# Optimization experiments

Hardware: AMD Instinct MI355X
Metric: run time of the kernel (lower is better)

The kernel has to match this reference:

```python
import jax, jax.numpy as jnp
import numpy as np

N = 100000      # nodes
E = 400000      # edges
G = 4096        # graphs in batch
ATOM_DIM = 101
BOND_DIM = 11
D = 128         # latent_dim
L = 3           # num_atom_layers
BN_EPS = 1e-5


def setup_inputs() -> dict:
    key = jax.random.key(0)
    ks = jax.random.split(key, 16)
    x = jax.random.normal(ks[0], (N, ATOM_DIM), dtype=jnp.float32)
    edge_index = jax.random.randint(ks[1], (2, E), 0, N, dtype=jnp.int64)
    batch = jnp.sort(jax.random.randint(ks[2], (N,), 0, G, dtype=jnp.int64))
    edge_attr = jax.random.normal(ks[3], (E, BOND_DIM), dtype=jnp.float32)
    s = 0.05
    embW = jax.random.normal(ks[4], (ATOM_DIM, D), dtype=jnp.float32) * s
    embB = jnp.zeros((D,), dtype=jnp.float32)
    bondW = jax.random.normal(ks[5], (L, BOND_DIM, D), dtype=jnp.float32) * s
    bondB = jnp.zeros((L, D), dtype=jnp.float32)
    W1 = jax.random.normal(ks[6], (L, D, 2 * D), dtype=jnp.float32) * s
    b1 = jnp.zeros((L, 2 * D), dtype=jnp.float32)
    g1 = jnp.ones((L, 2 * D), dtype=jnp.float32)
    be1 = jnp.zeros((L, 2 * D), dtype=jnp.float32)
    W2 = jax.random.normal(ks[7], (L, 2 * D, D), dtype=jnp.float32) * s
    b2 = jnp.zeros((L, D), dtype=jnp.float32)
    gout = jnp.ones((L, D), dtype=jnp.float32)
    bout = jnp.zeros((L, D), dtype=jnp.float32)
    return dict(x=x, edge_attr=edge_attr, embW=embW, embB=embB,
                bondW=bondW, bondB=bondB, W1=W1, b1=b1, g1=g1, be1=be1,
                W2=W2, b2=b2, gout=gout, bout=bout,
                edge_index=edge_index, batch=batch)


def _bn(h, gamma, beta):
    # BatchNorm1d in training mode: batch stats over node axis, biased variance
    m = h.mean(axis=0)
    v = h.var(axis=0)
    return (h - m) * jax.lax.rsqrt(v + BN_EPS) * gamma + beta


def reference(x, edge_attr, embW, embB, bondW, bondB, W1, b1, g1, be1,
              W2, b2, gout, bout, edge_index, batch):
    src, dst = edge_index[0], edge_index[1]
    h = x @ embW + embB                              # [N, D]
    for i in range(L):
        e = edge_attr @ bondW[i] + bondB[i]          # [E, D] bond embedding
        msg = jax.nn.relu(h[src] + e)                # gather + add + relu
        agg = jax.ops.segment_sum(msg, dst, num_segments=N)  # scatter-add
        z = h + agg                                  # (1 + eps) * x + agg, eps = 0
        z = jax.nn.relu(_bn(z @ W1[i] + b1[i], g1[i], be1[i]))  # [N, 2D]
        h = z @ W2[i] + b2[i]                        # [N, D]
        h = _bn(h, gout[i], bout[i])
        if i != L - 1:
            h = jax.nn.relu(h)
    # global mean pool per graph
    sums = jax.ops.segment_sum(h, batch, num_segments=G)            # [G, D]
    cnts = jax.ops.segment_sum(jnp.ones((h.shape[0],), h.dtype), batch,
                               num_segments=G)
    return sums / jnp.maximum(cnts, 1.0)[:, None]
```

## Files before the change

kernel.cpp:

```cpp
#include <hip/hip_runtime.h>
#include <hip/hip_bf16.h>

#define NN 100000
#define EE 400000
#define GG 4096
#define DD 128
#define ATOM_DIM 101
#define BOND_DIM 11
#define EAP 12
#define GEMM_GRID 512

typedef __attribute__((ext_vector_type(8))) short bf16x8;
typedef __attribute__((ext_vector_type(4))) float f32x4;
typedef __attribute__((ext_vector_type(2))) float f32x2;

__device__ __forceinline__ float b2f(short s) {
    unsigned u = ((unsigned)(unsigned short)s) << 16;
    float f; __builtin_memcpy(&f, &u, 4); return f;
}
__device__ __forceinline__ unsigned short f2b(float f) {
    unsigned u; __builtin_memcpy(&u, &f, 4);
    u += 0x7FFFu + ((u >> 16) & 1u);
    return (unsigned short)(u >> 16);
}

__global__ void detect64_kernel(const void* ei, int npairs, int* flag) {
    const int* p = (const int*)ei;
    int any = 0;
    for (int i = 1; i < 2 * npairs; i += 2) any |= p[i];
    *flag = (any == 0) ? 1 : 0;
}
__device__ __forceinline__ int getIdx(const void* p, long i, int is64) {
    if (is64) return (int)(((const long long*)p)[i]);
    return ((const int*)p)[i];
}

__global__ __launch_bounds__(256) void hist_kernel(
    const void* __restrict__ eidx, const int* __restrict__ flag, int* __restrict__ counts) {
    int e = blockIdx.x * 256 + threadIdx.x;
    if (e >= EE) return;
    int is64 = *flag;
    int dn = getIdx(eidx, (long)EE + e, is64);
    atomicAdd(&counts[dn], 1);
}

__global__ __launch_bounds__(256) void scan1_kernel(
    const int* __restrict__ counts, int* __restrict__ tmp, int* __restrict__ bsum, int n) {
    __shared__ int sd[256];
    const int tid = threadIdx.x;
    int i = blockIdx.x * 256 + tid;
    int v = (i < n) ? counts[i] : 0;
    sd[tid] = v; __syncthreads();
    #pragma unroll
    for (int off = 1; off < 256; off <<= 1) {
        int a = (tid >= off) ? sd[tid - off] : 0;
        __syncthreads();
        sd[tid] += a;
        __syncthreads();
    }
    if (i < n) tmp[i] = sd[tid] - v;
    if (tid == 255) bsum[blockIdx.x] = sd[255];
}

__global__ __launch_bounds__(512) void scan2_kernel(
    const int* __restrict__ bsum, int* __restrict__ bsumx, int nb) {
    __shared__ int sd[512];
    const int tid = threadIdx.x;
    int v = (tid < nb) ? bsum[tid] : 0;
    sd[tid] = v; __syncthreads();
    #pragma unroll
    for (int off = 1; off < 512; off <<= 1) {
        int a = (tid >= off) ? sd[tid - off] : 0;
        __syncthreads();
        sd[tid] += a;
        __syncthreads();
    }
    if (tid < nb) bsumx[tid] = sd[tid] - v;
}

__global__ __launch_bounds__(256) void scan3_kernel(
    const int* __restrict__ tmp, const int* __restrict__ bsumx,
    int* __restrict__ row_ptr, int n) {
    int i = blockIdx.x * 256 + threadIdx.x;
    if (i < n) row_ptr[i] = tmp[i] + bsumx[blockIdx.x];
    if (i == 0) row_ptr[n] = EE;
}

__global__ __launch_bounds__(256) void scatter_kernel(
    const void* __restrict__ eidx, const int* __restrict__ flag,
    const float* __restrict__ ea, const int* __restrict__ row_ptr,
    int* __restrict__ cursor, int* __restrict__ src_sorted, float* __restrict__ eas) {
    int e = blockIdx.x * 256 + threadIdx.x;
    if (e >= EE) return;
    int is64 = *flag;
    int dn = getIdx(eidx, (long)EE + e, is64);
    int sv = getIdx(eidx, e, is64);
    int pos = row_ptr[dn] + atomicAdd(&cursor[dn], 1);
    src_sorted[pos] = sv;
    const float* sp = ea + (long)e * BOND_DIM;
    float* dp = eas + (long)pos * EAP;
    #pragma unroll
    for (int k = 0; k < BOND_DIM; ++k) dp[k] = sp[k];
    dp[11] = 0.f;
}

#define EDGE_MATH(TV, EVp, A0, A1)                                              \
    {                                                                           \
        float c0 = bbv.x, c1 = bbv.y;                                           \
        _Pragma("unroll")                                                       \
        for (int k = 0; k < BOND_DIM; ++k) {                                    \
            c0 = fmaf((EVp)[k], wk0[k], c0);                                    \
            c1 = fmaf((EVp)[k], wk1[k], c1);                                    \
        }                                                                       \
        float f0 = b2f((short)((TV) & 0xffff)), f1 = b2f((short)((TV) >> 16));  \
        if (aff) { f0 = fmaxf(f0 * sc0 + sh0, 0.f); f1 = fmaxf(f1 * sc1v + sh1v, 0.f); } \
        A0 += fmaxf(f0 + c0, 0.f);                                              \
        A1 += fmaxf(f1 + c1, 0.f);                                              \
    }

__global__ __launch_bounds__(256) void msg_csr_kernel(
    const unsigned short* __restrict__ h,
    const float* __restrict__ sc, const float* __restrict__ sh,
    const int* __restrict__ src_sorted, const int* __restrict__ row_ptr,
    const float* __restrict__ eas,
    const float* __restrict__ bw,
    const float* __restrict__ bb,
    unsigned short* __restrict__ sout)
{
    const int tid = threadIdx.x;
    const int wave = tid >> 6, lane = tid & 63;
    const int d0 = lane * 2;
    float wk0[BOND_DIM], wk1[BOND_DIM];
    #pragma unroll
    for (int k = 0; k < BOND_DIM; ++k) {
        f32x2 wv = *(const f32x2*)(bw + k * DD + d0);
        wk0[k] = wv.x; wk1[k] = wv.y;
    }
    f32x2 bbv = *(const f32x2*)(bb + d0);
    const bool aff = (sc != nullptr);
    float sc0 = 1.f, sc1v = 1.f, sh0 = 0.f, sh1v = 0.f;
    if (aff) { sc0 = sc[d0]; sc1v = sc[d0 + 1]; sh0 = sh[d0]; sh1v = sh[d0 + 1]; }

    for (int n0 = blockIdx.x * 4 + wave; n0 < NN; n0 += gridDim.x * 4) {
        const int n = __builtin_amdgcn_readfirstlane(n0);
        const int e0 = __builtin_amdgcn_readfirstlane(row_ptr[n]);
        const int e1 = __builtin_amdgcn_readfirstlane(row_ptr[n + 1]);
        float a0 = 0.f, a1 = 0.f;
        int e = e0;
        for (; e + 4 <= e1; e += 4) {
            const int eu = __builtin_amdgcn_readfirstlane(e);
            int sv0 = __builtin_amdgcn_readfirstlane(src_sorted[eu]);
            int sv1 = __builtin_amdgcn_readfirstlane(src_sorted[eu + 1]);
            int sv2 = __builtin_amdgcn_readfirstlane(src_sorted[eu + 2]);
            int sv3 = __builtin_amdgcn_readfirstlane(src_sorted[eu + 3]);
            unsigned tv0 = *(const unsigned*)(h + (long)sv0 * DD + d0);
            unsigned tv1 = *(const unsigned*)(h + (long)sv1 * DD + d0);
            unsigned tv2 = *(const unsigned*)(h + (long)sv2 * DD + d0);
            unsigned tv3 = *(const unsigned*)(h + (long)sv3 * DD + d0);
            const float* ep0 = eas + (long)eu * EAP;
            EDGE_MATH(tv0, ep0, a0, a1)
            EDGE_MATH(tv1, ep0 + EAP, a0, a1)
            EDGE_MATH(tv2, ep0 + 2 * EAP, a0, a1)
            EDGE_MATH(tv3, ep0 + 3 * EAP, a0, a1)
        }
        if (e + 2 <= e1) {
            const int eu = __builtin_amdgcn_readfirstlane(e);
            int sv0 = __builtin_amdgcn_readfirstlane(src_sorted[eu]);
            int sv1 = __builtin_amdgcn_readfirstlane(src_sorted[eu + 1]);
            unsigned tv0 = *(const unsigned*)(h + (long)sv0 * DD + d0);
            unsigned tv1 = *(const unsigned*)(h + (long)sv1 * DD + d0);
            const float* ep0 = eas + (long)eu * EAP;
            EDGE_MATH(tv0, ep0, a0, a1)
            EDGE_MATH(tv1, ep0 + EAP, a0, a1)
            e += 2;
        }
        if (e < e1) {
            const int eu = __builtin_amdgcn_readfirstlane(e);
            int sv = __builtin_amdgcn_readfirstlane(src_sorted[eu]);
            unsigned tv = *(const unsigned*)(h + (long)sv * DD + d0);
            const float* ep0 = eas + (long)eu * EAP;
            EDGE_MATH(tv, ep0, a0, a1)
        }
        unsigned tn = *(const unsigned*)(h + (long)n * DD + d0);
        float t0 = b2f((short)(tn & 0xffff)), t1 = b2f((short)(tn >> 16));
        if (aff) {
            t0 = fmaxf(t0 * sc0 + sh0, 0.f); t1 = fmaxf(t1 * sc1v + sh1v, 0.f);
        }
        unsigned pk = (unsigned)f2b(t0 + a0) | ((unsigned)f2b(t1 + a1) << 16);
        *(unsigned*)(sout + (long)n * DD + d0) = pk;
    }
}

__global__ void pack_w(const float* __restrict__ W, unsigned short* __restrict__ Wf,
                       int Kact, int N, int KSTEPS) {
    int idx = blockIdx.x * blockDim.x + threadIdx.x;
    int NF = N >> 4;
    int total = KSTEPS * NF * 64;
    if (idx >= total) return;
    int l = idx & 63;
    int f = (idx >> 6) % NF;
    int ks = idx / (64 * NF);
    int col = f * 16 + (l & 15);
    int k0 = ks * 32 + (l >> 4) * 8;
    bf16x8 v;
    #pragma unroll
    for (int j = 0; j < 8; ++j) {
        int k = k0 + j;
        v[j] = (k < Kact) ? (short)f2b(W[(long)k * N + col]) : (short)0;
    }
    *(bf16x8*)(Wf + (long)idx * 8) = v;
}

__global__ void pack_x(const float* __restrict__ x, unsigned short* __restrict__ xb) {
    const long total = (long)NN * 128;
    for (long i = (long)blockIdx.x * blockDim.x + threadIdx.x; i < total;
         i += (long)gridDim.x * blockDim.x) {
        int col = (int)(i & 127);
        long row = i >> 7;
        xb[i] = (col < ATOM_DIM) ? f2b(x[row * ATOM_DIM + col]) : (unsigned short)0;
    }
}

template<int NF, int KSTEPS, int NHALVES, int MODE, bool OUT_BF16, bool STATS>
__global__ __launch_bounds__(256, 2) void gemm_reg(
    const unsigned short* __restrict__ A,
    const float* __restrict__ sc, const float* __restrict__ sh,
    const unsigned short* __restrict__ Wf,
    const float* __restrict__ bias,
    void* __restrict__ outp,
    float* __restrict__ partial,
    int M)
{
    constexpr int K = KSTEPS * 32;
    constexpr int NCb = NF * 16;
    constexpr int NFtot = NF * NHALVES;
    constexpr int NCtot = NCb * NHALVES;
    constexpr int ESZ = OUT_BF16 ? 2 : 4;
    constexpr int RSTRIDE = NCb + (OUT_BF16 ? 8 : 4);
    constexpr int ROWBYTES = NCb * ESZ;
    constexpr int CHUNKS = 64 * ROWBYTES / 16;
    constexpr int CPR = ROWBYTES / 16;

    __shared__ __align__(16) char sOut[64 * RSTRIDE * ESZ];
    __shared__ float s_sc[(MODE == 2) ? K : 1];
    __shared__ float s_sh[(MODE == 2) ? K : 1];
    __shared__ float s_ps[STATS ? 2 * NCb : 1];

    const int tid = threadIdx.x;
    const int wave = tid >> 6, l = tid & 63;
    const int kg = (l >> 4) * 8;

    int half, mt;
    if (NHALVES == 2) {
        int b = blockIdx.x;
        half = (b >> 3) & 1;
        mt = (b & 7) | ((b >> 4) << 3);
    } else {
        half = 0; mt = blockIdx.x;
    }
    const int col0 = half * NCb;
    const int bstep = gridDim.x / NHALVES;

    if (MODE == 2 || STATS) {
        if (MODE == 2) {
            for (int i = tid; i < K; i += 256) { s_sc[i] = sc[i]; s_sh[i] = sh[i]; }
        }
        if (STATS) {
            for (int i = tid; i < 2 * NCb; i += 256) s_ps[i] = 0.f;
        }
        __syncthreads();
    }

    bf16x8 bfr[KSTEPS][NF];
    {
        const bf16x8* wp = (const bf16x8*)Wf;
        #pragma unroll
        for (int ks = 0; ks < KSTEPS; ++ks)
            #pragma unroll
            for (int f = 0; f < NF; ++f)
                bfr[ks][f] = wp[((long)ks * NFtot + half * NF + f) * 64 + l];
    }

    float bb[NF];
    #pragma unroll
    for (int f = 0; f < NF; ++f) bb[f] = bias[col0 + f * 16 + (l & 15)];

    float ssum[NF], ssq[NF];
    #pragma unroll
    for (int f = 0; f < NF; ++f) { ssum[f] = 0.f; ssq[f] = 0.f; }

    const int MT = (M + 63) >> 6;

    bf16x8 ldA[KSTEPS], ldB[KSTEPS];
    {
        int rr = mt * 64 + wave * 16 + (l & 15);
        int rc = rr < M ? rr : M - 1;
        const unsigned short* ap = A + (long)rc * K + kg;
        #pragma unroll
        for (int ks = 0; ks < KSTEPS; ++ks) ldA[ks] = *(const bf16x8*)(ap + ks * 32);
    }

    for (; mt < MT; mt += bstep) {
        const int nxt = mt + bstep;
        if (nxt < MT) {
            int rr = nxt * 64 + wave * 16 + (l & 15);
            int rc = rr < M ? rr : M - 1;
            const unsigned short* ap = A + (long)rc * K + kg;
            #pragma unroll
            for (int ks = 0; ks < KSTEPS; ++ks) ldB[ks] = *(const bf16x8*)(ap + ks * 32);
        }

        if (MODE == 2) {
            #pragma unroll
            for (int ks = 0; ks < KSTEPS; ++ks) {
                f32x4 s0 = *(const f32x4*)&s_sc[ks * 32 + kg];
                f32x4 s1 = *(const f32x4*)&s_sc[ks * 32 + kg + 4];
                f32x4 h0 = *(const f32x4*)&s_sh[ks * 32 + kg];
                f32x4 h1 = *(const f32x4*)&s_sh[ks * 32 + kg + 4];
                float sv[8] = {s0.x, s0.y, s0.z, s0.w, s1.x, s1.y, s1.z, s1.w};
                float hv[8] = {h0.x, h0.y, h0.z, h0.w, h1.x, h1.y, h1.z, h1.w};
                #pragma unroll
                for (int j = 0; j < 8; ++j) {
                    float v = fmaxf(b2f(ldA[ks][j]) * sv[j] + hv[j], 0.f);
                    ldA[ks][j] = (short)f2b(v);
                }
            }
        }

        f32x4 acc[NF];
        #pragma unroll
        for (int f = 0; f < NF; ++f) acc[f] = (f32x4){0.f, 0.f, 0.f, 0.f};
        #pragma unroll
        for (int ks = 0; ks < KSTEPS; ++ks)
            #pragma unroll
            for (int f = 0; f < NF; ++f)
                acc[f] = __builtin_amdgcn_mfma_f32_16x16x32_bf16(ldA[ks], bfr[ks][f], acc[f], 0, 0, 0);

        const int rtile = mt * 64;
        #pragma unroll
        for (int f = 0; f < NF; ++f) {
            const int cl = f * 16 + (l & 15);
            #pragma unroll
            for (int j = 0; j < 4; ++j) {
                const int rl = wave * 16 + (l >> 4) * 4 + j;
                float v = acc[f][j] + bb[f];
                if (OUT_BF16) ((unsigned short*)sOut)[rl * RSTRIDE + cl] = f2b(v);
                else          ((float*)sOut)[rl * RSTRIDE + cl] = v;
                if (STATS && rtile + rl < M) { ssum[f] += v; ssq[f] += v * v; }
            }
        }
        __syncthreads();

        const int rmax = M - rtile;
        #pragma unroll
        for (int i = 0; i < CHUNKS / 256; ++i) {
            int c = i * 256 + tid;
            int row = c / CPR;
            int off = (c % CPR) * 16;
            if (row < rmax) {
                f32x4 v = *(const f32x4*)(sOut + row * (RSTRIDE * ESZ) + off);
                char* gp = (char*)outp + ((long)(rtile + row) * NCtot + col0) * ESZ + off;
                *(f32x4*)gp = v;
            }
        }
        __syncthreads();

        #pragma unroll
        for (int ks = 0; ks < KSTEPS; ++ks) ldA[ks] = ldB[ks];
    }

    if (STATS) {
        #pragma unroll
        for (int f = 0; f < NF; ++f) {
            float s = ssum[f], q = ssq[f];
            s += __shfl_xor(s, 16); s += __shfl_xor(s, 32);
            q += __shfl_xor(q, 16); q += __shfl_xor(q, 32);
            if (l < 16) {
                atomicAdd(&s_ps[f * 16 + l], s);
                atomicAdd(&s_ps[NCb + f * 16 + l], q);
            }
        }
        __syncthreads();
        float* pb = partial + (long)blockIdx.x * 2 * NCb;
        for (int i = tid; i < 2 * NCb; i += 256) pb[i] = s_ps[i];
    }
}

__global__ __launch_bounds__(64) void bn_finalize_p(
    const float* __restrict__ partial, int nblk, int ncb, int halves,
    const float* __restrict__ gamma, const float* __restrict__ beta,
    float invN, float* __restrict__ sc, float* __restrict__ sh)
{
    const int c = blockIdx.x;
    const int t = threadIdx.x;
    float s = 0.f, q = 0.f;
    for (int b = t; b < nblk; b += 64) {
        int half = (halves == 2) ? ((b >> 3) & 1) : 0;
        if (c / ncb != half) continue;
        const float* pb = partial + (long)b * 2 * ncb;
        s += pb[c % ncb];
        q += pb[ncb + c % ncb];
    }
    #pragma unroll
    for (int off = 1; off < 64; off <<= 1) {
        s += __shfl_xor(s, off);
        q += __shfl_xor(q, off);
    }
    if (t == 0) {
        float m = s * invN;
        float v = q * invN - m * m;
        float g = gamma[c] * rsqrtf(v + 1e-5f);
        sc[c] = g;
        sh[c] = beta[c] - m * g;
    }
}

__global__ __launch_bounds__(64) void pool_kernel(
    const unsigned short* __restrict__ h,
    const float* __restrict__ sc, const float* __restrict__ sh,
    const void* __restrict__ batchp, const int* __restrict__ flag,
    int Nn, float* __restrict__ out)
{
    const int g = blockIdx.x;
    const int t = threadIdx.x;
    const int d0 = t * 2;
    const int is64 = *flag;
    int lo = 0, hi = Nn;
    while (lo < hi) { int mid = (lo + hi) >> 1; if (getIdx(batchp, mid, is64) < g) lo = mid + 1; else hi = mid; }
    const int s0 = lo;
    hi = Nn;
    while (lo < hi) { int mid = (lo + hi) >> 1; if (getIdx(batchp, mid, is64) < g + 1) lo = mid + 1; else hi = mid; }
    const int s1 = lo;
    float a0 = 0.f, a1 = 0.f;
    for (int r = s0; r < s1; ++r) {
        unsigned v = *(const unsigned*)(h + (long)r * DD + d0);
        a0 += b2f((short)(v & 0xffff));
        a1 += b2f((short)(v >> 16));
    }
    const int cnt = s1 - s0;
    f32x2 o; o.x = 0.f; o.y = 0.f;
    if (cnt > 0) {
        float inv = 1.f / (float)cnt;
        o.x = a0 * inv * sc[d0] + sh[d0];
        o.y = a1 * inv * sc[d0 + 1] + sh[d0 + 1];
    }
    *(f32x2*)(out + (long)g * DD + d0) = o;
}

extern "C" void kernel_launch(void* const* d_in, const int* in_sizes, int n_in,
                              void* d_out, int out_size, void* d_ws, size_t ws_size,
                              hipStream_t stream)
{
    const float* x     = (const float*)d_in[0];
    const float* ea    = (const float*)d_in[1];
    const float* embW  = (const float*)d_in[2];
    const float* embB  = (const float*)d_in[3];
    const float* bondW = (const float*)d_in[4];
    const float* bondB = (const float*)d_in[5];
    const float* W1    = (const float*)d_in[6];
    const float* b1    = (const float*)d_in[7];
    const float* g1    = (const float*)d_in[8];
    const float* be1   = (const float*)d_in[9];
    const float* W2    = (const float*)d_in[10];
    const float* b2    = (const float*)d_in[11];
    const float* gout  = (const float*)d_in[12];
    const float* bout  = (const float*)d_in[13];
    const void*  eidx  = d_in[14];
    const void*  batch = d_in[15];
    float* out = (float*)d_out;

    char* w = (char*)d_ws;
    unsigned short* h   = (unsigned short*)w;   w += (long)NN * DD * 2;
    unsigned short* s   = (unsigned short*)w;   w += (long)NN * DD * 2;
    unsigned short* z1  = (unsigned short*)w;   w += (long)NN * 256 * 2;
    unsigned short* xb  = z1;
    float* eas  = (float*)w;                    w += (long)EE * EAP * 4;
    int* src_sorted = (int*)w;                  w += (long)EE * 4;
    int* row_ptr    = (int*)w;                  w += (long)(NN + 1) * 4;
    int* counts     = (int*)w;                  w += (long)NN * 4;
    int* tmp        = (int*)w;                  w += (long)NN * 4;
    int* bsum       = (int*)w;                  w += 1024 * 4;
    int* bsumx      = (int*)w;                  w += 1024 * 4;
    float* partial  = (float*)w;                w += (long)GEMM_GRID * 512 * 4;
    float* sc1  = (float*)w;                    w += 256 * 4;
    float* sh1  = (float*)w;                    w += 256 * 4;
    float* sc2  = (float*)w;                    w += 128 * 4;
    float* sh2  = (float*)w;                    w += 128 * 4;
    unsigned short* embWf = (unsigned short*)w; w += 4 * 8  * 64 * 8 * 2;
    unsigned short* W1f   = (unsigned short*)w; w += 3L * 4 * 16 * 64 * 8 * 2;
    unsigned short* W2f   = (unsigned short*)w; w += 3L * 8 * 8  * 64 * 8 * 2;
    int* flag = (int*)w;

    detect64_kernel<<<1, 1, 0, stream>>>(eidx, 256, flag);

    pack_x<<<4096, 256, 0, stream>>>(x, xb);
    pack_w<<<8, 256, 0, stream>>>(embW, embWf, ATOM_DIM, 128, 4);
    for (int i = 0; i < 3; ++i) {
        pack_w<<<16, 256, 0, stream>>>(W1 + (long)i * 128 * 256, W1f + (long)i * 4 * 16 * 64 * 8, 128, 256, 4);
        pack_w<<<16, 256, 0, stream>>>(W2 + (long)i * 256 * 128, W2f + (long)i * 8 * 8 * 64 * 8, 256, 128, 8);
    }

    const int eblocks = (EE + 255) / 256;
    const int nb = (NN + 255) / 256;
    hipMemsetAsync(counts, 0, (size_t)NN * 4, stream);
    hist_kernel<<<eblocks, 256, 0, stream>>>(eidx, flag, counts);
    scan1_kernel<<<nb, 256, 0, stream>>>(counts, tmp, bsum, NN);
    scan2_kernel<<<1, 512, 0, stream>>>(bsum, bsumx, nb);
    scan3_kernel<<<nb, 256, 0, stream>>>(tmp, bsumx, row_ptr, NN);
    hipMemsetAsync(counts, 0, (size_t)NN * 4, stream);
    scatter_kernel<<<eblocks, 256, 0, stream>>>(eidx, flag, ea, row_ptr, counts, src_sorted, eas);

    gemm_reg<8, 4, 1, 0, true, false><<<GEMM_GRID, 256, 0, stream>>>(
        xb, nullptr, nullptr, embWf, embB, h, nullptr, NN);

    const float* scin = nullptr;
    const float* shin = nullptr;

    for (int i = 0; i < 3; ++i) {
        msg_csr_kernel<<<4096, 256, 0, stream>>>(
            h, scin, shin, src_sorted, row_ptr, eas,
            bondW + (long)i * BOND_DIM * DD, bondB + (long)i * DD, s);

        gemm_reg<8, 4, 2, 0, true, true><<<GEMM_GRID, 256, 0, stream>>>(
            s, nullptr, nullptr, W1f + (long)i * 4 * 16 * 64 * 8,
            b1 + (long)i * 256, z1, partial, NN);
        bn_finalize_p<<<256, 64, 0, stream>>>(partial, GEMM_GRID, 128, 2,
            g1 + (long)i * 256, be1 + (long)i * 256, 1.f / NN, sc1, sh1);

        gemm_reg<4, 8, 2, 2, true, true><<<GEMM_GRID, 256, 0, stream>>>(
            z1, sc1, sh1, W2f + (long)i * 8 * 8 * 64 * 8,
            b2 + (long)i * DD, h, partial, NN);
        bn_finalize_p<<<128, 64, 0, stream>>>(partial, GEMM_GRID, 64, 2,
            gout + (long)i * DD, bout + (long)i * DD, 1.f / NN, sc2, sh2);

        scin = sc2; shin = sh2;
    }

    pool_kernel<<<GG, 64, 0, stream>>>(h, sc2, sh2, batch, flag, NN, out);
}
```

Baseline: 475.7 us.

## Fuse x packing into embedding GEMM, double-buffer output staging, parallelize detect

Removes the separate pack_x kernel: the embedding GEMM now reads fp32 x directly and converts it to bf16 in registers, with zero padding past ATOM_DIM. This drops one full write and read of a padded bf16 copy of x. The LDS output staging buffer is doubled so the second __syncthreads per tile can be removed, and the detect64 kernel now runs on 256 threads instead of one. The in-register conversion uses scalar, unaligned fp32 loads (row stride 101), so the loads are less coalesced than the previous 16-byte vector loads.

```diff
diff --git a/kernel.cpp b/kernel.cpp
--- a/kernel.cpp
+++ b/kernel.cpp
@@ -25,10 +25,15 @@
 }
 
 __global__ void detect64_kernel(const void* ei, int npairs, int* flag) {
+    __shared__ int any;
+    if (threadIdx.x == 0) any = 0;
+    __syncthreads();
     const int* p = (const int*)ei;
-    int any = 0;
-    for (int i = 1; i < 2 * npairs; i += 2) any |= p[i];
-    *flag = (any == 0) ? 1 : 0;
+    int v = 0;
+    for (int i = threadIdx.x; i < npairs; i += blockDim.x) v |= p[2 * i + 1];
+    if (v) atomicOr(&any, 1);
+    __syncthreads();
+    if (threadIdx.x == 0) *flag = (any == 0) ? 1 : 0;
 }
 __device__ __forceinline__ int getIdx(const void* p, long i, int is64) {
     if (is64) return (int)(((const long long*)p)[i]);
@@ -211,19 +216,30 @@
     *(bf16x8*)(Wf + (long)idx * 8) = v;
 }
 
-__global__ void pack_x(const float* __restrict__ x, unsigned short* __restrict__ xb) {
-    const long total = (long)NN * 128;
-    for (long i = (long)blockIdx.x * blockDim.x + threadIdx.x; i < total;
-         i += (long)gridDim.x * blockDim.x) {
-        int col = (int)(i & 127);
-        long row = i >> 7;
-        xb[i] = (col < ATOM_DIM) ? f2b(x[row * ATOM_DIM + col]) : (unsigned short)0;
-    }
-}
-
-template<int NF, int KSTEPS, int NHALVES, int MODE, bool OUT_BF16, bool STATS>
+template<int MODE, int KSTEPS, int KACT>
+__device__ __forceinline__ void loadA(const void* Ap, long rc, int kg, bf16x8* dst) {
+    if (MODE == 1) {
+        const float* ap = (const float*)Ap + rc * KACT;
+        #pragma unroll
+        for (int ks = 0; ks < KSTEPS; ++ks) {
+            bf16x8 a;
+            #pragma unroll
+            for (int j = 0; j < 8; ++j) {
+                int gk = ks * 32 + kg + j;
+                a[j] = (gk < KACT) ? (short)f2b(ap[gk]) : (short)0;
+            }
+            dst[ks] = a;
+        }
+    } else {
+        const unsigned short* ap = (const unsigned short*)Ap + rc * (KSTEPS * 32) + kg;
+        #pragma unroll
+        for (int ks = 0; ks < KSTEPS; ++ks) dst[ks] = *(const bf16x8*)(ap + ks * 32);
+    }
+}
+
+template<int NF, int KSTEPS, int NHALVES, int MODE, bool OUT_BF16, bool STATS, int KACT = 0>
 __global__ __launch_bounds__(256, 2) void gemm_reg(
-    const unsigned short* __restrict__ A,
+    const void* __restrict__ Ap,
     const float* __restrict__ sc, const float* __restrict__ sh,
     const unsigned short* __restrict__ Wf,
     const float* __restrict__ bias,
@@ -241,7 +257,7 @@
     constexpr int CHUNKS = 64 * ROWBYTES / 16;
     constexpr int CPR = ROWBYTES / 16;
 
-    __shared__ __align__(16) char sOut[64 * RSTRIDE * ESZ];
+    __shared__ __align__(16) char sOut[2][64 * RSTRIDE * ESZ];
     __shared__ float s_sc[(MODE == 2) ? K : 1];
     __shared__ float s_sh[(MODE == 2) ? K : 1];
     __shared__ float s_ps[STATS ? 2 * NCb : 1];
@@ -295,19 +311,16 @@
     {
         int rr = mt * 64 + wave * 16 + (l & 15);
         int rc = rr < M ? rr : M - 1;
-        const unsigned short* ap = A + (long)rc * K + kg;
-        #pragma unroll
-        for (int ks = 0; ks < KSTEPS; ++ks) ldA[ks] = *(const bf16x8*)(ap + ks * 32);
-    }
-
+        loadA<MODE, KSTEPS, KACT>(Ap, rc, kg, ldA);
+    }
+
+    int pbuf = 0;
     for (; mt < MT; mt += bstep) {
         const int nxt = mt + bstep;
         if (nxt < MT) {
             int rr = nxt * 64 + wave * 16 + (l & 15);
             int rc = rr < M ? rr : M - 1;
-            const unsigned short* ap = A + (long)rc * K + kg;
-            #pragma unroll
-            for (int ks = 0; ks < KSTEPS; ++ks) ldB[ks] = *(const bf16x8*)(ap + ks * 32);
+            loadA<MODE, KSTEPS, KACT>(Ap, rc, kg, ldB);
         }
 
         if (MODE == 2) {
@@ -337,6 +350,7 @@
                 acc[f] = __builtin_amdgcn_mfma_f32_16x16x32_bf16(ldA[ks], bfr[ks][f], acc[f], 0, 0, 0);
 
         const int rtile = mt * 64;
+        char* sb = sOut[pbuf];
         #pragma unroll
         for (int f = 0; f < NF; ++f) {
             const int cl = f * 16 + (l & 15);
@@ -344,8 +358,8 @@
             for (int j = 0; j < 4; ++j) {
                 const int rl = wave * 16 + (l >> 4) * 4 + j;
                 float v = acc[f][j] + bb[f];
-                if (OUT_BF16) ((unsigned short*)sOut)[rl * RSTRIDE + cl] = f2b(v);
-                else          ((float*)sOut)[rl * RSTRIDE + cl] = v;
+                if (OUT_BF16) ((unsigned short*)sb)[rl * RSTRIDE + cl] = f2b(v);
+                else          ((float*)sb)[rl * RSTRIDE + cl] = v;
                 if (STATS && rtile + rl < M) { ssum[f] += v; ssq[f] += v * v; }
             }
         }
@@ -358,12 +372,12 @@
             int row = c / CPR;
             int off = (c % CPR) * 16;
             if (row < rmax) {
-                f32x4 v = *(const f32x4*)(sOut + row * (RSTRIDE * ESZ) + off);
+                f32x4 v = *(const f32x4*)(sb + row * (RSTRIDE * ESZ) + off);
                 char* gp = (char*)outp + ((long)(rtile + row) * NCtot + col0) * ESZ + off;
                 *(f32x4*)gp = v;
             }
         }
-        __syncthreads();
+        pbuf ^= 1;
 
         #pragma unroll
         for (int ks = 0; ks < KSTEPS; ++ks) ldA[ks] = ldB[ks];
@@ -473,7 +487,6 @@
     unsigned short* h   = (unsigned short*)w;   w += (long)NN * DD * 2;
     unsigned short* s   = (unsigned short*)w;   w += (long)NN * DD * 2;
     unsigned short* z1  = (unsigned short*)w;   w += (long)NN * 256 * 2;
-    unsigned short* xb  = z1;
     float* eas  = (float*)w;                    w += (long)EE * EAP * 4;
     int* src_sorted = (int*)w;                  w += (long)EE * 4;
     int* row_ptr    = (int*)w;                  w += (long)(NN + 1) * 4;
@@ -491,9 +504,8 @@
     unsigned short* W2f   = (unsigned short*)w; w += 3L * 8 * 8  * 64 * 8 * 2;
     int* flag = (int*)w;
 
-    detect64_kernel<<<1, 1, 0, stream>>>(eidx, 256, flag);
-
-    pack_x<<<4096, 256, 0, stream>>>(x, xb);
+    detect64_kernel<<<1, 256, 0, stream>>>(eidx, 256, flag);
+
     pack_w<<<8, 256, 0, stream>>>(embW, embWf, ATOM_DIM, 128, 4);
     for (int i = 0; i < 3; ++i) {
         pack_w<<<16, 256, 0, stream>>>(W1 + (long)i * 128 * 256, W1f + (long)i * 4 * 16 * 64 * 8, 128, 256, 4);
@@ -510,8 +522,8 @@
     hipMemsetAsync(counts, 0, (size_t)NN * 4, stream);
     scatter_kernel<<<eblocks, 256, 0, stream>>>(eidx, flag, ea, row_ptr, counts, src_sorted, eas);
 
-    gemm_reg<8, 4, 1, 0, true, false><<<GEMM_GRID, 256, 0, stream>>>(
-        xb, nullptr, nullptr, embWf, embB, h, nullptr, NN);
+    gemm_reg<8, 4, 1, 1, true, false, ATOM_DIM><<<GEMM_GRID, 256, 0, stream>>>(
+        x, nullptr, nullptr, embWf, embB, h, nullptr, NN);
 
     const float* scin = nullptr;
     const float* shin = nullptr;
```

After: 451.0 us. 1.05x faster.
